# Kernel tuning notes

Hardware: AMD Instinct MI355X
Metric: run time of the kernel (lower is better)

The kernel has to match this reference:

```python
import jax, jax.numpy as jnp
import numpy as np

T, B = 128, 256
E, H, C = 128, 1024, 10
VOCAB = 10


def setup_inputs() -> dict:
    key = jax.random.key(0)
    ks = jax.random.split(key, 12)
    x = jax.random.randint(ks[0], (T, B), 0, VOCAB)
    emb = jax.random.normal(ks[1], (VOCAB, E), dtype=jnp.float32)
    Wgx = jax.random.normal(ks[2], (E, H), dtype=jnp.float32) / np.sqrt(E)
    Wgh = jax.random.normal(ks[3], (H, H), dtype=jnp.float32) / np.sqrt(H)
    Wix = jax.random.normal(ks[4], (E, H), dtype=jnp.float32) / np.sqrt(E)
    Wih = jax.random.normal(ks[5], (H, H), dtype=jnp.float32) / np.sqrt(H)
    Wfx = jax.random.normal(ks[6], (E, H), dtype=jnp.float32) / np.sqrt(E)
    Wfh = jax.random.normal(ks[7], (H, H), dtype=jnp.float32) / np.sqrt(H)
    Wox = jax.random.normal(ks[8], (E, H), dtype=jnp.float32) / np.sqrt(E)
    Woh = jax.random.normal(ks[9], (H, H), dtype=jnp.float32) / np.sqrt(H)
    Wph = jax.random.normal(ks[10], (H, C), dtype=jnp.float32) / np.sqrt(H)
    bg = jnp.zeros((H,), jnp.float32)
    bi = jnp.zeros((H,), jnp.float32)
    bf = jnp.zeros((H,), jnp.float32)
    bo = jnp.zeros((H,), jnp.float32)
    bp = jnp.zeros((C,), jnp.float32)
    return dict(x=x, emb=emb, Wgx=Wgx, Wgh=Wgh, Wix=Wix, Wih=Wih, Wfx=Wfx,
                Wfh=Wfh, Wox=Wox, Woh=Woh, bg=bg, bi=bi, bf=bf, bo=bo,
                Wph=Wph, bp=bp)


def reference(x, emb, Wgx, Wgh, Wix, Wih, Wfx, Wfh, Wox, Woh,
              bg, bi, bf, bo, Wph, bp):
    Bsz = x.shape[1]
    Hn = Wgh.shape[0]
    # Fuse the 8 gate matmuls into 2 GEMMs per step (same math, concat order g,i,f,o)
    Wx = jnp.concatenate([Wgx, Wix, Wfx, Wox], axis=1)  # [E, 4H]
    Wh = jnp.concatenate([Wgh, Wih, Wfh, Woh], axis=1)  # [H, 4H]
    b = jnp.concatenate([bg, bi, bf, bo], axis=0)        # [4H]

    def step(carry, xt):
        state, hidden = carry
        e = emb[xt]                                      # [B, E]
        pre = e @ Wx + hidden @ Wh + b                   # [B, 4H]
        g = jnp.tanh(pre[:, :Hn])
        i = jax.nn.sigmoid(pre[:, Hn:2 * Hn])
        f = jax.nn.sigmoid(pre[:, 2 * Hn:3 * Hn])
        o = jax.nn.sigmoid(pre[:, 3 * Hn:])
        state = g * i + state * f
        hidden = jnp.tanh(state) * o
        return (state, hidden), None

    init = (jnp.zeros((Bsz, Hn), jnp.float32), jnp.zeros((Bsz, Hn), jnp.float32))
    (state, hidden), _ = jax.lax.scan(step, init, x)
    # Original detaches hidden/state before the output projection
    hidden = jax.lax.stop_gradient(hidden)
    return hidden @ Wph + bp                             # [B, C]
```

## Files before the change

kernel.cpp:

```cpp
#include <hip/hip_runtime.h>

typedef __bf16 bf16;
typedef __bf16 bf16x8 __attribute__((ext_vector_type(8)));
typedef float  f32x4  __attribute__((ext_vector_type(4)));
typedef int    i32x4  __attribute__((ext_vector_type(4)));

#define T_STEPS 128
#define BATCH   256
#define HD      1024
#define N4H     4096
#define EMB_D   128

#define MFMA_BF16(acc, Aop, Bop) \
    asm("v_mfma_f32_16x16x32_bf16 %0, %1, %2, %0" : "+v"(acc) : "a"(Aop), "v"(Bop))

__device__ __forceinline__ float fast_sigmoid(float x) {
    return 1.0f / (1.0f + __expf(-x));
}
__device__ __forceinline__ float fast_tanh(float x) {
    return 1.0f - 2.0f / (__expf(2.0f * x) + 1.0f);
}

__global__ void build_P(const float* __restrict__ emb,
                        const float* __restrict__ Wgx, const float* __restrict__ Wix,
                        const float* __restrict__ Wfx, const float* __restrict__ Wox,
                        const float* __restrict__ bg,  const float* __restrict__ bi,
                        const float* __restrict__ bfv, const float* __restrict__ bo,
                        float* __restrict__ P)
{
    int n = blockIdx.x * 256 + threadIdx.x;
    int v  = n >> 12;
    int nn = n & (N4H - 1);
    int hcol = nn >> 2, gate = nn & 3;
    const float* Wx = (gate == 0) ? Wgx : (gate == 1) ? Wix : (gate == 2) ? Wfx : Wox;
    const float* bb = (gate == 0) ? bg  : (gate == 1) ? bi  : (gate == 2) ? bfv : bo;
    float s = bb[hcol];
    for (int e = 0; e < EMB_D; ++e)
        s += emb[v * EMB_D + e] * Wx[e * HD + hcol];
    P[n] = s;
}

__global__ void build_W(const float* __restrict__ Wgh, const float* __restrict__ Wih,
                        const float* __restrict__ Wfh, const float* __restrict__ Woh,
                        bf16* __restrict__ WhpT)
{
    __shared__ float tile[64][65];
    int bid  = blockIdx.x;
    int gate = bid >> 8;
    int t2   = bid & 255;
    int kt = t2 >> 4, ht = t2 & 15;
    const float* W = (gate == 0) ? Wgh : (gate == 1) ? Wih : (gate == 2) ? Wfh : Woh;
    int tid = threadIdx.x;
    #pragma unroll
    for (int it = 0; it < 16; ++it) {
        int idx = it * 256 + tid;
        int kk = idx >> 6, hh = idx & 63;
        tile[kk][hh] = W[(size_t)(kt * 64 + kk) * HD + ht * 64 + hh];
    }
    __syncthreads();
    #pragma unroll
    for (int it = 0; it < 16; ++it) {
        int idx = it * 256 + tid;
        int hh = idx >> 6, kk = idx & 63;
        int n = (ht * 64 + hh) * 4 + gate;
        WhpT[(size_t)n * HD + kt * 64 + kk] = (bf16)tile[kk][hh];
    }
}

__global__ __launch_bounds__(512, 2)
void lstm_main(const int* __restrict__ x, const float* __restrict__ P,
               const bf16* __restrict__ WhpT, bf16* __restrict__ hbuf,
               int* __restrict__ ctl)
{
    __shared__ bf16  Blds[32][1024];
    __shared__ float red[8][64][9];
    __shared__ bf16  hst[32][34];
    __shared__ int   sj;

    const int tid  = threadIdx.x;
    const int lane = tid & 63;
    const int wid  = tid >> 6;
    const int w    = wid & 3;
    const int kh   = wid >> 2;
    const int frow = lane & 15;
    const int kgrp = lane >> 4;

    int xcc;
    asm("s_getreg_b32 %0, hwreg(HW_REG_XCC_ID)" : "=s"(xcc));
    const int g = xcc & 7;
    if (tid == 0)
        sj = __hip_atomic_fetch_add(ctl + 1024 + g * 16, 1,
                                    __ATOMIC_RELAXED, __HIP_MEMORY_SCOPE_AGENT) & 31;
    __syncthreads();
    const int j = sj;
    int* bar = ctl + g * 128;

    const int rowO = j * 128 + w * 32 + kh * 16 + frow;
    const int rowX = j * 128 + w * 32 + (1 - kh) * 16 + frow;
    const bf16* AbO = WhpT + (size_t)rowO * HD + kh * 512 + kgrp * 8;
    const bf16* AbX = WhpT + (size_t)rowX * HD + kh * 512 + kgrp * 8;
    i32x4 ArO[16], ArX[16];
    #pragma unroll
    for (int ks = 0; ks < 16; ++ks) {
        ArO[ks] = *(const i32x4*)(const void*)(AbO + ks * 32);
        ArX[ks] = *(const i32x4*)(const void*)(AbX + ks * 32);
    }
    #pragma unroll
    for (int ks = 0; ks < 16; ++ks)
        asm volatile("" : "+a"(ArO[ks]), "+a"(ArX[ks]));

    const int mr0 = g * 32 + frow;
    const int clc = w * 8 + kh * 4 + kgrp;
    const int pnb = j * 128 + clc * 4;
    const int xorf = frow & 7;
    char* BB = (char*)&Blds[0][0];
    float* rw = &red[0][0][0] + ((size_t)(wid ^ 4) * 64 + lane) * 9;
    const float* rr = &red[0][0][0] + ((size_t)wid * 64 + lane) * 9;

    float st0 = 0.f, st1 = 0.f;
    f32x4 accP0, accP1;
    {
        int xv0 = x[mr0], xv1 = x[mr0 + 16];
        accP0 = *(const f32x4*)(P + (size_t)xv0 * N4H + pnb);
        accP1 = *(const f32x4*)(P + (size_t)xv1 * N4H + pnb);
    }

    for (int t = 0; t < T_STEPS; ++t) {
        f32x4 accO0 = accP0, accO1 = accP1;
        f32x4 z = {0.f, 0.f, 0.f, 0.f};
        f32x4 accX0 = z, accX1 = z;

        if (t > 0) {
            if (tid == 0) {
                const int tgt = 32 * t;
                long guard = 0;
                int sum;
                do {
                    sum = 0;
                    #pragma unroll
                    for (int s8 = 0; s8 < 8; ++s8)
                        sum += __hip_atomic_load(bar + s8 * 16, __ATOMIC_RELAXED,
                                                 __HIP_MEMORY_SCOPE_AGENT);
                } while (sum < tgt && ++guard < (1L << 22));
            }
            __syncthreads();
            const char* src = (const char*)(hbuf + (size_t)(t & 1) * BATCH * HD
                                                 + (size_t)g * 32 * HD);
            f32x4 stg[8];
            #pragma unroll
            for (int i2 = 0; i2 < 8; ++i2)
                asm volatile("global_load_dwordx4 %0, %1, off sc0"
                             : "=v"(stg[i2]) : "v"(src + (i2 * 512 + tid) * 16));
            asm volatile("s_waitcnt vmcnt(0)" ::: "memory");
            #pragma unroll
            for (int i2 = 0; i2 < 8; ++i2) {
                int c = i2 * 512 + tid;
                int row = c >> 7, cg = c & 127;
                *(f32x4*)(BB + row * 2048 + ((cg ^ (row & 7)) << 4)) = stg[i2];
            }
            __syncthreads();
            #pragma unroll
            for (int ks = 0; ks < 16; ++ks) {
                int off = ((kh * 64 + ks * 4 + kgrp) ^ xorf) << 4;
                i32x4 b0 = *(const i32x4*)(BB + frow * 2048 + off);
                i32x4 b1 = *(const i32x4*)(BB + (frow + 16) * 2048 + off);
                MFMA_BF16(accO0, ArO[ks], b0);
                MFMA_BF16(accO1, ArO[ks], b1);
                MFMA_BF16(accX0, ArX[ks], b0);
                MFMA_BF16(accX1, ArX[ks], b1);
            }
        }

        rw[0] = accX0[0]; rw[1] = accX0[1]; rw[2] = accX0[2]; rw[3] = accX0[3];
        rw[4] = accX1[0]; rw[5] = accX1[1]; rw[6] = accX1[2]; rw[7] = accX1[3];
        __syncthreads();
        accO0[0] += rr[0]; accO0[1] += rr[1]; accO0[2] += rr[2]; accO0[3] += rr[3];
        accO1[0] += rr[4]; accO1[1] += rr[5]; accO1[2] += rr[6]; accO1[3] += rr[7];

        {
            float gg = fast_tanh(accO0[0]);
            float ii = fast_sigmoid(accO0[1]);
            float ff = fast_sigmoid(accO0[2]);
            float oo = fast_sigmoid(accO0[3]);
            float s = gg * ii + st0 * ff;
            st0 = s;
            hst[frow][clc] = (bf16)(fast_tanh(s) * oo);
        }
        {
            float gg = fast_tanh(accO1[0]);
            float ii = fast_sigmoid(accO1[1]);
            float ff = fast_sigmoid(accO1[2]);
            float oo = fast_sigmoid(accO1[3]);
            float s = gg * ii + st1 * ff;
            st1 = s;
            hst[frow + 16][clc] = (bf16)(fast_tanh(s) * oo);
        }

        if (t < T_STEPS - 1) {
            int xv0 = x[(t + 1) * BATCH + mr0], xv1 = x[(t + 1) * BATCH + mr0 + 16];
            accP0 = *(const f32x4*)(P + (size_t)xv0 * N4H + pnb);
            accP1 = *(const f32x4*)(P + (size_t)xv1 * N4H + pnb);
        }

        __syncthreads();
        {
            bf16* hout = hbuf + (size_t)((t + 1) & 1) * BATCH * HD;
            int r = tid >> 4, cp = (tid & 15) * 2;
            unsigned lo = (unsigned)__builtin_bit_cast(unsigned short, hst[r][cp]);
            unsigned hi = (unsigned)__builtin_bit_cast(unsigned short, hst[r][cp + 1]);
            unsigned pv = lo | (hi << 16);
            *(unsigned*)(hout + (size_t)(g * 32 + r) * HD + j * 32 + cp) = pv;
        }
        __syncthreads();
        if (tid == 0 && t < T_STEPS - 1)
            __hip_atomic_fetch_add(bar + (j & 7) * 16, 1,
                                   __ATOMIC_RELAXED, __HIP_MEMORY_SCOPE_AGENT);
    }
}

__global__ void proj_out(const bf16* __restrict__ h, const float* __restrict__ Wph,
                         const float* __restrict__ bp, float* __restrict__ out)
{
    __shared__ float red[256][10];
    int b = blockIdx.x, tid = threadIdx.x;
    float acc[10];
    #pragma unroll
    for (int c = 0; c < 10; ++c) acc[c] = 0.f;
    for (int k = tid; k < HD; k += 256) {
        float hv = (float)h[(size_t)b * HD + k];
        #pragma unroll
        for (int c = 0; c < 10; ++c)
            acc[c] += hv * Wph[k * 10 + c];
    }
    #pragma unroll
    for (int c = 0; c < 10; ++c) red[tid][c] = acc[c];
    __syncthreads();
    for (int s = 128; s > 0; s >>= 1) {
        if (tid < s) {
            #pragma unroll
            for (int c = 0; c < 10; ++c) red[tid][c] += red[tid + s][c];
        }
        __syncthreads();
    }
    if (tid < 10) out[b * 10 + tid] = red[0][tid] + bp[tid];
}

extern "C" void kernel_launch(void* const* d_in, const int* in_sizes, int n_in,
                              void* d_out, int out_size, void* d_ws, size_t ws_size,
                              hipStream_t stream)
{
    const int*   x   = (const int*)  d_in[0];
    const float* emb = (const float*)d_in[1];
    const float* Wgx = (const float*)d_in[2];
    const float* Wgh = (const float*)d_in[3];
    const float* Wix = (const float*)d_in[4];
    const float* Wih = (const float*)d_in[5];
    const float* Wfx = (const float*)d_in[6];
    const float* Wfh = (const float*)d_in[7];
    const float* Wox = (const float*)d_in[8];
    const float* Woh = (const float*)d_in[9];
    const float* bg  = (const float*)d_in[10];
    const float* bi  = (const float*)d_in[11];
    const float* bfv = (const float*)d_in[12];
    const float* bo  = (const float*)d_in[13];
    const float* Wph = (const float*)d_in[14];
    const float* bp  = (const float*)d_in[15];

    char* ws = (char*)d_ws;
    bf16*  WhpT = (bf16*)ws;
    float* P    = (float*)(ws + 8388608);
    bf16*  hbuf = (bf16*)(ws + 8388608 + 163840);
    int*   ctl  = (int*)(ws + 8388608 + 163840 + 1048576);

    hipMemsetAsync(ctl, 0, 8192, stream);
    build_P<<<160, 256, 0, stream>>>(emb, Wgx, Wix, Wfx, Wox, bg, bi, bfv, bo, P);
    build_W<<<1024, 256, 0, stream>>>(Wgh, Wih, Wfh, Woh, WhpT);

    void* args[] = { (void*)&x, (void*)&P, (void*)&WhpT, (void*)&hbuf, (void*)&ctl };
    hipLaunchCooperativeKernel((void*)lstm_main, dim3(256), dim3(512), args, 0, stream);

    proj_out<<<256, 256, 0, stream>>>(hbuf, Wph, bp, (float*)d_out);
}
```

Measured before the change: 519.3 us.

## Load hidden-state fragments directly from global memory instead of staging in LDS

Each step no longer cooperatively copies the 32x1024 bf16 hidden slice into swizzled LDS with a block barrier. Each lane instead loads its MFMA B fragments straight from global memory and prefetches the next k-slice one iteration ahead. An acquire load is added after the spin barrier so the plain loads see fresh data. A 64KB dynamic shared allocation, touched only under a never-true condition, keeps LDS usage unchanged. This removes one __syncthreads and the LDS round trip, at the cost of redundant L2 traffic across waves and exposed global latency on the recurrent critical path.

```diff
diff --git a/kernel.cpp b/kernel.cpp
--- a/kernel.cpp
+++ b/kernel.cpp
@@ -72,7 +72,7 @@
                const bf16* __restrict__ WhpT, bf16* __restrict__ hbuf,
                int* __restrict__ ctl)
 {
-    __shared__ bf16  Blds[32][1024];
+    extern __shared__ char dynpad[];
     __shared__ float red[8][64][9];
     __shared__ bf16  hst[32][34];
     __shared__ int   sj;
@@ -84,6 +84,8 @@
     const int kh   = wid >> 2;
     const int frow = lane & 15;
     const int kgrp = lane >> 4;
+
+    if (blockDim.y == 2) dynpad[tid] = 1;
 
     int xcc;
     asm("s_getreg_b32 %0, hwreg(HW_REG_XCC_ID)" : "=s"(xcc));
@@ -112,8 +114,6 @@
     const int mr0 = g * 32 + frow;
     const int clc = w * 8 + kh * 4 + kgrp;
     const int pnb = j * 128 + clc * 4;
-    const int xorf = frow & 7;
-    char* BB = (char*)&Blds[0][0];
     float* rw = &red[0][0][0] + ((size_t)(wid ^ 4) * 64 + lane) * 9;
     const float* rr = &red[0][0][0] + ((size_t)wid * 64 + lane) * 9;
 
@@ -142,32 +142,27 @@
                         sum += __hip_atomic_load(bar + s8 * 16, __ATOMIC_RELAXED,
                                                  __HIP_MEMORY_SCOPE_AGENT);
                 } while (sum < tgt && ++guard < (1L << 22));
+                (void)__hip_atomic_load(bar, __ATOMIC_ACQUIRE,
+                                        __HIP_MEMORY_SCOPE_AGENT);
             }
             __syncthreads();
-            const char* src = (const char*)(hbuf + (size_t)(t & 1) * BATCH * HD
-                                                 + (size_t)g * 32 * HD);
-            f32x4 stg[8];
-            #pragma unroll
-            for (int i2 = 0; i2 < 8; ++i2)
-                asm volatile("global_load_dwordx4 %0, %1, off sc0"
-                             : "=v"(stg[i2]) : "v"(src + (i2 * 512 + tid) * 16));
-            asm volatile("s_waitcnt vmcnt(0)" ::: "memory");
-            #pragma unroll
-            for (int i2 = 0; i2 < 8; ++i2) {
-                int c = i2 * 512 + tid;
-                int row = c >> 7, cg = c & 127;
-                *(f32x4*)(BB + row * 2048 + ((cg ^ (row & 7)) << 4)) = stg[i2];
-            }
-            __syncthreads();
+            const bf16* hin = hbuf + (size_t)(t & 1) * BATCH * HD;
+            const bf16* Br0 = hin + (size_t)mr0 * HD + kh * 512 + kgrp * 8;
+            const bf16* Br1 = Br0 + (size_t)16 * HD;
+            i32x4 c0 = *(const i32x4*)(const void*)Br0;
+            i32x4 c1 = *(const i32x4*)(const void*)Br1;
             #pragma unroll
             for (int ks = 0; ks < 16; ++ks) {
-                int off = ((kh * 64 + ks * 4 + kgrp) ^ xorf) << 4;
-                i32x4 b0 = *(const i32x4*)(BB + frow * 2048 + off);
-                i32x4 b1 = *(const i32x4*)(BB + (frow + 16) * 2048 + off);
-                MFMA_BF16(accO0, ArO[ks], b0);
-                MFMA_BF16(accO1, ArO[ks], b1);
-                MFMA_BF16(accX0, ArX[ks], b0);
-                MFMA_BF16(accX1, ArX[ks], b1);
+                i32x4 n0, n1;
+                if (ks < 15) {
+                    n0 = *(const i32x4*)(const void*)(Br0 + (ks + 1) * 32);
+                    n1 = *(const i32x4*)(const void*)(Br1 + (ks + 1) * 32);
+                }
+                MFMA_BF16(accO0, ArO[ks], c0);
+                MFMA_BF16(accO1, ArO[ks], c1);
+                MFMA_BF16(accX0, ArX[ks], c0);
+                MFMA_BF16(accX1, ArX[ks], c1);
+                c0 = n0; c1 = n1;
             }
         }
 
@@ -277,7 +272,7 @@
     build_W<<<1024, 256, 0, stream>>>(Wgh, Wih, Wfh, Woh, WhpT);
 
     void* args[] = { (void*)&x, (void*)&P, (void*)&WhpT, (void*)&hbuf, (void*)&ctl };
-    hipLaunchCooperativeKernel((void*)lstm_main, dim3(256), dim3(512), args, 0, stream);
+    hipLaunchCooperativeKernel((void*)lstm_main, dim3(256), dim3(512), args, 65536, stream);
 
     proj_out<<<256, 256, 0, stream>>>(hbuf, Wph, bp, (float*)d_out);
 }
```

Result: slower. 1.416 ms (+172.6%).
